# Kernel tuning notes

Measured on AMD Instinct MI355X. Metric: run time of the kernel, lower is better.

## Reference

```python
import jax, jax.numpy as jnp
import numpy as np

N = 128          # n_nodes (hardcoded groups=128 in the torch module)
TIME_DIM = 16
XYZ_DIM = 63
SIGMA = 0.3
EPS = 0.01
relu = jax.nn.relu


def gconv(x, W, b):
    # grouped 1x1 Conv1d with groups=N: per-node GEMM
    # x: (N, Cin, L), W: (N, Cout, Cin), b: (N, Cout) -> (N, Cout, L)
    return jnp.einsum('ncl,nkc->nkl', x, W) + b[:, :, None]


def setup_inputs() -> dict:
    key = jax.random.key(0)
    ks = iter(jax.random.split(key, 64))

    def W(shape, fan_in):
        return jax.random.normal(next(ks), shape, jnp.float32) / np.float32(np.sqrt(fan_in))

    def bvec(shape):
        return 0.01 * jax.random.normal(next(ks), shape, jnp.float32)

    B, V = 1, 2048
    inp = {
        'poses': 0.1 * jax.random.normal(next(ks), (B, N, 24, 3), jnp.float32),
        't_ped': jax.random.normal(next(ks), (B, TIME_DIM), jnp.float32),
        'w': jax.random.uniform(next(ks), (N, 24), jnp.float32),
        'wpts': jax.random.uniform(next(ks), (B, V, 3), jnp.float32),
        'nodes_posed': jax.random.uniform(next(ks), (B, N, 3), jnp.float32),
        'local_coords': jax.random.normal(next(ks), (N, B, V, XYZ_DIM), jnp.float32),
        # encoder grouped convs
        'Wec1': W((N, 64, 72 + TIME_DIM), 72 + TIME_DIM), 'bec1': bvec((N, 64)),
        'Wec21': W((N, 8, 64), 64), 'bec21': bvec((N, 8)),
        'Wec22': W((N, 8, 64), 64), 'bec22': bvec((N, 8)),
        # decoder grouped convs
        'Wdc1': W((N, 64, 80), 80), 'bdc1': bvec((N, 64)),
        'Wdc21': W((N, 32, 64), 64), 'bdc21': bvec((N, 32)),
        'Wdc22': W((N, 3, 64), 64), 'bdc22': bvec((N, 3)),
        # feature-field grouped convs
        'Wf1': W((N, 64, 32 + XYZ_DIM), 32 + XYZ_DIM), 'bf1': bvec((N, 64)),
        'Wf2': W((N, 64, 64), 64), 'bf2': bvec((N, 64)),
        'Wf3': W((N, 64, 64), 64), 'bf3': bvec((N, 64)),
        'Wf4': W((N, 256, 64), 64), 'bf4': bvec((N, 256)),
        # Nerf head linears
        'Wc1': W((256, 64), 256), 'bc1': bvec((64,)),
        'Wc2': W((64, 3), 64), 'bc2': bvec((3,)),
        'Wd1': W((256, 1), 256), 'bd1': bvec((1,)),
    }
    return inp


def reference(poses, t_ped, w, wpts, nodes_posed, local_coords,
              Wec1, bec1, Wec21, bec21, Wec22, bec22,
              Wdc1, bdc1, Wdc21, bdc21, Wdc22, bdc22,
              Wf1, bf1, Wf2, bf2, Wf3, bf3, Wf4, bf4,
              Wc1, bc1, Wc2, bc2, Wd1, bd1):
    B, V = poses.shape[0], wpts.shape[1]

    # attention-weighted poses: (B, N, 72)
    poses_w = (w[None, :, :, None] * poses).reshape(B, N, 72)

    # ---- encode ----
    t = jnp.broadcast_to(t_ped[:, None, :], (B, N, TIME_DIM))
    enc_in = jnp.concatenate([poses_w, t], axis=-1).transpose(1, 2, 0)   # (N, 72+td, B)
    net = relu(gconv(enc_in, Wec1, bec1))                                # (N, 64, B)
    mean = gconv(net, Wec21, bec21).transpose(0, 2, 1)                   # (N, B, 8)
    logvar = gconv(net, Wec22, bec22).transpose(0, 2, 1)                 # (N, B, 8)
    z = mean  # eval-mode reparameterize

    # ---- decode ----
    dec_in = jnp.concatenate([poses_w, z.transpose(1, 0, 2)], axis=-1).transpose(1, 2, 0)  # (N, 80, B)
    net = relu(gconv(dec_in, Wdc1, bdc1))
    ei = gconv(net, Wdc21, bdc21).transpose(0, 2, 1)                     # (N, B, 32)
    delta_ni = gconv(net, Wdc22, bdc22).transpose(0, 2, 1)               # (N, B, 3)

    # ---- blend weights: RBF influence of each node on each point ----
    diff = wpts[None, :, :, :] - nodes_posed.transpose(1, 0, 2)[:, :, None, :]  # (N, B, V, 3)
    d2 = jnp.sum(diff * diff, axis=-1)                                   # (N, B, V)
    influ = jnp.exp(-d2 / (2.0 * SIGMA * SIGMA)) - EPS
    mask = influ >= 0
    bweights = jnp.maximum(influ, 0.0)

    # ---- feature field (dense per-node MLP, masked; == padded gather/scatter) ----
    raw = jnp.concatenate([jnp.broadcast_to(ei[:, :, None, :], (N, B, V, 32)),
                           local_coords], axis=-1)                       # (N, B, V, 32+xyz)
    x = raw.reshape(N, B * V, 32 + XYZ_DIM).transpose(0, 2, 1)           # (N, Cin, B*V)
    net = relu(gconv(x, Wf1, bf1))
    net = relu(gconv(net, Wf2, bf2))
    net = relu(gconv(net, Wf3, bf3))
    fout = relu(gconv(net, Wf4, bf4))                                    # (N, 256, B*V)
    f = fout.transpose(0, 2, 1).reshape(N, B, V, 256) * mask[..., None].astype(fout.dtype)

    # ---- blend features ----
    bw = bweights.transpose(1, 2, 0) + 1e-7                              # (B, V, N)
    bw = bw / jnp.sum(bw, axis=-1, keepdims=True)
    f_blend = jnp.einsum('nbvc,bvn->bvc', f, bw)                         # (B, V, 256)

    # ---- Nerf head ----
    netc = relu(f_blend @ Wc1 + bc1)
    c = netc @ Wc2 + bc2                                                 # (B, V, 3)
    d = relu(f_blend @ Wd1 + bd1)                                        # (B, V, 1)
    return (c, d, ei, delta_ni, mean, logvar)
```

## Files before the change

### kernel.cpp

```cpp
#include <hip/hip_runtime.h>

typedef __bf16 bf16;
typedef __bf16 bf16x4 __attribute__((ext_vector_type(4)));
typedef float  f32x4  __attribute__((ext_vector_type(4)));
typedef unsigned short u16x4 __attribute__((ext_vector_type(4)));

#define NPTS 2048
#define LD 68
#define XCC_ID_IMM 63508

__global__ __launch_bounds__(256) void k_sniff(const void* poses_raw, int* flag)
{
    __shared__ int cnt;
    if (threadIdx.x == 0) cnt = 0;
    __syncthreads();
    const bf16* pb = (const bf16*)poses_raw;
    int local = 0;
    for (int i = threadIdx.x; i < 9216; i += 256) {
        float v = (float)pb[i];
        if (!(v >= -2.0f && v <= 2.0f)) local++;
    }
    atomicAdd(&cnt, local);
    __syncthreads();
    if (threadIdx.x == 0) *flag = (cnt < 64) ? 1 : 0;
}

template<typename T, int WANT>
__global__ __launch_bounds__(128) void k_encdec_t(
    const T* __restrict__ poses, const T* __restrict__ t_ped, const T* __restrict__ w,
    const T* __restrict__ Wec1, const T* __restrict__ bec1,
    const T* __restrict__ Wec21, const T* __restrict__ bec21,
    const T* __restrict__ Wec22, const T* __restrict__ bec22,
    const T* __restrict__ Wdc1, const T* __restrict__ bdc1,
    const T* __restrict__ Wdc21, const T* __restrict__ bdc21,
    const T* __restrict__ Wdc22, const T* __restrict__ bdc22,
    T* __restrict__ out_ei, T* __restrict__ out_delta,
    T* __restrict__ out_mean, T* __restrict__ out_logvar,
    const int* __restrict__ flag)
{
    if (*flag != WANT) return;
    int n = blockIdx.x, tid = threadIdx.x;
    __shared__ float sin_[88], zbuf[8], net1[64], din[80], net2[64];
    if (tid < 72)      sin_[tid] = (float)w[n*24 + tid/3] * (float)poses[n*72 + tid];
    else if (tid < 88) sin_[tid] = (float)t_ped[tid - 72];
    __syncthreads();
    if (tid < 64) {
        float a = (float)bec1[n*64 + tid];
        const T* wr = Wec1 + (size_t)(n*64 + tid) * 88;
        for (int c = 0; c < 88; ++c) a += (float)wr[c] * sin_[c];
        net1[tid] = fmaxf(a, 0.f);
    }
    __syncthreads();
    if (tid < 8) {
        float a = (float)bec21[n*8 + tid];
        const T* wr = Wec21 + (size_t)(n*8 + tid) * 64;
        for (int c = 0; c < 64; ++c) a += (float)wr[c] * net1[c];
        out_mean[n*8 + tid] = (T)a;
        zbuf[tid] = a;
    } else if (tid < 16) {
        int o = tid - 8;
        float a = (float)bec22[n*8 + o];
        const T* wr = Wec22 + (size_t)(n*8 + o) * 64;
        for (int c = 0; c < 64; ++c) a += (float)wr[c] * net1[c];
        out_logvar[n*8 + o] = (T)a;
    }
    __syncthreads();
    if (tid < 72)      din[tid] = sin_[tid];
    else if (tid < 80) din[tid] = zbuf[tid - 72];
    __syncthreads();
    if (tid < 64) {
        float a = (float)bdc1[n*64 + tid];
        const T* wr = Wdc1 + (size_t)(n*64 + tid) * 80;
        for (int c = 0; c < 80; ++c) a += (float)wr[c] * din[c];
        net2[tid] = fmaxf(a, 0.f);
    }
    __syncthreads();
    if (tid < 32) {
        float a = (float)bdc21[n*32 + tid];
        const T* wr = Wdc21 + (size_t)(n*32 + tid) * 64;
        for (int c = 0; c < 64; ++c) a += (float)wr[c] * net2[c];
        out_ei[n*32 + tid] = (T)a;
    } else if (tid < 35) {
        int o = tid - 32;
        float a = (float)bdc22[n*3 + o];
        const T* wr = Wdc22 + (size_t)(n*3 + o) * 64;
        for (int c = 0; c < 64; ++c) a += (float)wr[c] * net2[c];
        out_delta[n*3 + o] = (T)a;
    }
}

template<typename T, int WANT>
__global__ __launch_bounds__(256) void k_denom(
    const T* __restrict__ wpts, const T* __restrict__ nodes,
    float* __restrict__ inv, const int* __restrict__ flag)
{
    if (*flag != WANT) return;
    int v = blockIdx.x * 256 + threadIdx.x;
    float px = (float)wpts[v*3+0], py = (float)wpts[v*3+1], pz = (float)wpts[v*3+2];
    float denom = 0.f;
    for (int n = 0; n < 128; ++n) {
        float dx = px - (float)nodes[n*3+0];
        float dy = py - (float)nodes[n*3+1];
        float dz = pz - (float)nodes[n*3+2];
        float d2 = dx*dx + dy*dy + dz*dz;
        float influ = expf(-d2 * (1.0f/0.18f)) - 0.01f;
        denom += fmaxf(influ, 0.f) + 1e-7f;
    }
    inv[v] = 1.f / denom;
}

__device__ __forceinline__ f32x4 ld4(const float* p) { return *(const f32x4*)p; }
__device__ __forceinline__ f32x4 ld4(const bf16* p)
{
    bf16x4 v = *(const bf16x4*)p;
    f32x4 r;
    #pragma unroll
    for (int j = 0; j < 4; ++j) r[j] = (float)v[j];
    return r;
}
__device__ __forceinline__ f32x4 ld4_nt(const float* p)
{
    return __builtin_nontemporal_load((const f32x4*)p);
}
__device__ __forceinline__ f32x4 ld4_nt(const bf16* p)
{
    u16x4 u = __builtin_nontemporal_load((const u16x4*)p);
    f32x4 r;
    #pragma unroll
    for (int j = 0; j < 4; ++j) {
        unsigned int bits = ((unsigned int)u[j]) << 16;
        r[j] = __uint_as_float(bits);
    }
    return r;
}

template<typename T, int WANT>
__global__ __launch_bounds__(256) void k_w1prep(
    const T* __restrict__ Wf1, float* __restrict__ W1p, const int* __restrict__ flag)
{
    if (*flag != WANT) return;
    int n = blockIdx.x, tid = threadIdx.x;
    for (int e = tid; e < 6144; e += 256) {
        int oc = e / 96, k = e - oc*96;
        float v = (k < 95) ? (float)Wf1[(size_t)n*6080 + oc*95 + k] : 0.f;
        W1p[(size_t)n*6144 + e] = v;
    }
}

template<typename T>
__device__ __forceinline__ void layer64g(
    const T* __restrict__ W, const T* __restrict__ b,
    const float* __restrict__ hin, float* __restrict__ hout, int og, int pg)
{
    f32x4 acc[4] = {};
    #pragma unroll 4
    for (int k0 = 0; k0 < 64; k0 += 4) {
        f32x4 wv[4], xv[4];
        #pragma unroll
        for (int c = 0; c < 4; ++c) wv[c] = ld4(W + (size_t)(og*4 + c)*64 + k0);
        #pragma unroll
        for (int j = 0; j < 4; ++j) xv[j] = *(const f32x4*)&hin[(k0 + j)*LD + pg*4];
        #pragma unroll
        for (int c = 0; c < 4; ++c)
            #pragma unroll
            for (int j = 0; j < 4; ++j)
                acc[c] += xv[j] * wv[c][j];
    }
    #pragma unroll
    for (int c = 0; c < 4; ++c) {
        float bb = (float)b[og*4 + c];
        f32x4 hv;
        #pragma unroll
        for (int r = 0; r < 4; ++r) hv[r] = fmaxf(acc[c][r] + bb, 0.f);
        *(f32x4*)&hout[(og*4 + c)*LD + pg*4] = hv;
    }
}

template<typename T, int WANT, int W1P>
__global__ __launch_bounds__(256, 3) void k_feat_fast(
    const T* __restrict__ Wf1, const T* __restrict__ Wf2,
    const T* __restrict__ Wf3, const T* __restrict__ Wf4,
    const T* __restrict__ lc, const T* __restrict__ ei,
    const T* __restrict__ bf1, const T* __restrict__ bf2,
    const T* __restrict__ bf3, const T* __restrict__ bf4,
    const T* __restrict__ wpts, const T* __restrict__ nodes,
    const float* __restrict__ inv, const float* __restrict__ W1p,
    int shift, float* __restrict__ slices,
    const int* __restrict__ flag)
{
    if (*flag != WANT) return;
    int bid = blockIdx.x;
    int xcdg = bid & 7;
    int i    = bid >> 3;
    int g     = 4*xcdg + (i >> 5);
    int ptile = i & 31;
    int p0  = ptile * 64;
    int tid = threadIdx.x;
    int og = tid >> 4;
    int pg = tid & 15;

    int xcdr = (__builtin_amdgcn_s_getreg(XCC_ID_IMM) & 7) >> shift;

    __shared__ __attribute__((aligned(16))) float smem[(96 + 64) * LD];
    float* xs = smem;
    float* hA = smem + 96*LD;

    if (tid < 64) xs[95*LD + tid] = 0.f;

    float px[4], py[4], pz[4], pinv[4];
    #pragma unroll
    for (int r = 0; r < 4; ++r) {
        int p = p0 + pg*4 + r;
        px[r] = (float)wpts[p*3+0];
        py[r] = (float)wpts[p*3+1];
        pz[r] = (float)wpts[p*3+2];
        pinv[r] = inv[p];
    }

    f32x4 fb[4][4];
    #pragma unroll
    for (int a = 0; a < 4; ++a)
        #pragma unroll
        for (int c = 0; c < 4; ++c) fb[a][c] = (f32x4){0.f,0.f,0.f,0.f};

    f32x4 lv[4];

    auto stage_load = [&](int n) {
        const T* src = lc + ((size_t)n*NPTS + p0) * 63;
        if (tid < 252) {
            #pragma unroll
            for (int j = 0; j < 4; ++j) lv[j] = ld4_nt(src + tid*16 + j*4);
        }
    };
    auto stage_write = [&](int n) {
        if (tid < 252) {
            #pragma unroll
            for (int j = 0; j < 4; ++j)
                #pragma unroll
                for (int l = 0; l < 4; ++l) {
                    int e = tid*16 + j*4 + l;
                    int p = e/63, c = e - 63*p;
                    xs[(32 + c)*LD + p] = lv[j][l];
                }
        }
        const T* ein = ei + n*32;
        #pragma unroll
        for (int k = 0; k < 8; ++k) {
            int e = k*256 + tid;
            int row = e >> 6, p = e & 63;
            xs[row*LD + p] = (float)ein[row];
        }
    };

    stage_load(g*4);
    stage_write(g*4);
    __syncthreads();

    #pragma unroll 1
    for (int nn = 0; nn < 4; ++nn) {
        int n = g*4 + nn;

        {
            f32x4 acc[4] = {};
            if (W1P) {
                const float* W1b = W1p + (size_t)(n*64 + og*4) * 96;
                #pragma unroll 4
                for (int k0 = 0; k0 < 96; k0 += 4) {
                    f32x4 wv[4], xv[4];
                    #pragma unroll
                    for (int c = 0; c < 4; ++c) wv[c] = ld4(W1b + (size_t)c*96 + k0);
                    #pragma unroll
                    for (int j = 0; j < 4; ++j) xv[j] = *(const f32x4*)&xs[(k0 + j)*LD + pg*4];
                    #pragma unroll
                    for (int c = 0; c < 4; ++c)
                        #pragma unroll
                        for (int j = 0; j < 4; ++j)
                            acc[c] += xv[j] * wv[c][j];
                }
            } else {
                const T* W1b = Wf1 + (size_t)(n*64 + og*4) * 95;
                #pragma unroll 4
                for (int kk = 0; kk < 23; ++kk) {
                    int k0 = kk*4;
                    float wv[4][4]; f32x4 xv[4];
                    #pragma unroll
                    for (int c = 0; c < 4; ++c) {
                        const T* wr = W1b + (size_t)c*95 + k0;
                        #pragma unroll
                        for (int j = 0; j < 4; ++j) wv[c][j] = (float)wr[j];
                    }
                    #pragma unroll
                    for (int j = 0; j < 4; ++j) xv[j] = *(const f32x4*)&xs[(k0 + j)*LD + pg*4];
                    #pragma unroll
                    for (int c = 0; c < 4; ++c)
                        #pragma unroll
                        for (int j = 0; j < 4; ++j)
                            acc[c] += xv[j] * wv[c][j];
                }
                {
                    f32x4 xt[3];
                    #pragma unroll
                    for (int j = 0; j < 3; ++j) xt[j] = *(const f32x4*)&xs[(92 + j)*LD + pg*4];
                    #pragma unroll
                    for (int c = 0; c < 4; ++c) {
                        const T* wr = W1b + (size_t)c*95;
                        #pragma unroll
                        for (int j = 0; j < 3; ++j)
                            acc[c] += xt[j] * (float)wr[92 + j];
                    }
                }
            }
            #pragma unroll
            for (int c = 0; c < 4; ++c) {
                float bb = (float)bf1[n*64 + og*4 + c];
                f32x4 hv;
                #pragma unroll
                for (int r = 0; r < 4; ++r) hv[r] = fmaxf(acc[c][r] + bb, 0.f);
                *(f32x4*)&hA[(og*4 + c)*LD + pg*4] = hv;
            }
        }
        __syncthreads();

        layer64g(Wf2 + (size_t)n*64*64, bf2 + n*64, hA, xs, og, pg);
        __syncthreads();

        layer64g(Wf3 + (size_t)n*64*64, bf3 + n*64, xs, hA, og, pg);
        __syncthreads();

        if (nn < 3) stage_load(n + 1);

        {
            float nx = (float)nodes[n*3+0], ny = (float)nodes[n*3+1], nz = (float)nodes[n*3+2];
            f32x4 wgtv;
            #pragma unroll
            for (int r = 0; r < 4; ++r) {
                float dx = px[r]-nx, dy = py[r]-ny, dz = pz[r]-nz;
                float d2 = dx*dx + dy*dy + dz*dz;
                float influ = expf(-d2 * (1.0f/0.18f)) - 0.01f;
                wgtv[r] = (influ >= 0.f) ? (fmaxf(influ, 0.f) + 1e-7f) * pinv[r] : 0.f;
            }
            const T* W4n = Wf4 + (size_t)n*256*64;
            const T* b4n = bf4 + n*256;
            #pragma unroll 1
            for (int mt = 0; mt < 4; ++mt) {
                f32x4 acc[4] = {};
                #pragma unroll 4
                for (int k0 = 0; k0 < 64; k0 += 4) {
                    f32x4 wv[4], xv[4];
                    #pragma unroll
                    for (int c = 0; c < 4; ++c)
                        wv[c] = ld4(W4n + (size_t)(mt*64 + og*4 + c)*64 + k0);
                    #pragma unroll
                    for (int j = 0; j < 4; ++j) xv[j] = *(const f32x4*)&hA[(k0 + j)*LD + pg*4];
                    #pragma unroll
                    for (int c = 0; c < 4; ++c)
                        #pragma unroll
                        for (int j = 0; j < 4; ++j)
                            acc[c] += xv[j] * wv[c][j];
                }
                #pragma unroll
                for (int c = 0; c < 4; ++c) {
                    float bb = (float)b4n[mt*64 + og*4 + c];
                    #pragma unroll
                    for (int r = 0; r < 4; ++r)
                        fb[mt][c][r] += fmaxf(acc[c][r] + bb, 0.f) * wgtv[r];
                }
            }
        }
        __syncthreads();
        if (nn < 3) { stage_write(n + 1); __syncthreads(); }
    }

    float* dst = slices + (size_t)xcdr * NPTS * 256;
    float* tbuf = smem;
    #pragma unroll 1
    for (int qq = 0; qq < 4; ++qq) {
        if (qq) __syncthreads();
        if ((pg >> 2) == qq) {
            #pragma unroll
            for (int mt = 0; mt < 4; ++mt)
                #pragma unroll
                for (int r = 0; r < 4; ++r) {
                    int row = (pg & 3)*4 + r;
                    f32x4 v = { fb[mt][0][r], fb[mt][1][r], fb[mt][2][r], fb[mt][3][r] };
                    *(f32x4*)&tbuf[row*260 + mt*64 + og*4] = v;
                }
        }
        __syncthreads();
        #pragma unroll
        for (int k = 0; k < 4; ++k) {
            int idx = k*1024 + tid*4;
            int row = idx >> 8, col = idx & 255;
            f32x4 v = *(const f32x4*)&tbuf[row*260 + col];
            size_t o = ((size_t)(p0 + qq*16 + row))*256 + col;
            #pragma unroll
            for (int j = 0; j < 4; ++j) atomicAdd(&dst[o + j], v[j]);
        }
    }
}

template<int WANT>
__global__ __launch_bounds__(256) void k_reduce(
    float* __restrict__ slices, int nslice, const int* __restrict__ flag)
{
    if (*flag != WANT) return;
    size_t t = (size_t)(blockIdx.x*256 + threadIdx.x) * 4;
    f32x4 s = *(const f32x4*)&slices[t];
    for (int gg = 1; gg < nslice; ++gg)
        s += __builtin_nontemporal_load((const f32x4*)&slices[(size_t)gg*NPTS*256 + t]);
    *(f32x4*)&slices[t] = s;
}

__global__ __launch_bounds__(256) void k_zero_fb(float* __restrict__ fb)
{
    fb[(size_t)blockIdx.x*256 + threadIdx.x] = 0.f;
}

template<typename T, int WANT>
__global__ __launch_bounds__(256) void k_head_t(
    const float* __restrict__ f_blend,
    const T* __restrict__ Wc1, const T* __restrict__ bc1,
    const T* __restrict__ Wc2, const T* __restrict__ bc2,
    const T* __restrict__ Wd1, const T* __restrict__ bd1,
    T* __restrict__ out_c, T* __restrict__ out_d,
    const int* __restrict__ flag)
{
    if (*flag != WANT) return;
    int t = blockIdx.x * 256 + threadIdx.x;
    int p = t >> 6, j = t & 63;
    const float* fb = f_blend + (size_t)p * 256;

    float a = (float)bc1[j];
    #pragma unroll 8
    for (int c = 0; c < 256; ++c)
        a += fb[c] * (float)Wc1[c*64 + j];
    float nc = fmaxf(a, 0.f);

    float s0 = nc * (float)Wc2[j*3 + 0];
    float s1 = nc * (float)Wc2[j*3 + 1];
    float s2 = nc * (float)Wc2[j*3 + 2];
    float sd = 0.f;
    #pragma unroll
    for (int u = 0; u < 4; ++u) {
        int c = j*4 + u;
        sd += fb[c] * (float)Wd1[c];
    }
    #pragma unroll
    for (int off = 32; off > 0; off >>= 1) {
        s0 += __shfl_down(s0, off);
        s1 += __shfl_down(s1, off);
        s2 += __shfl_down(s2, off);
        sd += __shfl_down(sd, off);
    }
    if (j == 0) {
        out_c[p*3 + 0] = (T)(s0 + (float)bc2[0]);
        out_c[p*3 + 1] = (T)(s1 + (float)bc2[1]);
        out_c[p*3 + 2] = (T)(s2 + (float)bc2[2]);
        out_d[p]       = (T)fmaxf(sd + (float)bd1[0], 0.f);
    }
}

extern "C" void kernel_launch(void* const* d_in, const int* in_sizes, int n_in,
                              void* d_out, int out_size, void* d_ws, size_t ws_size,
                              hipStream_t stream)
{
    const size_t SLICE_BYTES = (size_t)NPTS * 256 * 4;
    const size_t W1P_BYTES   = (size_t)128 * 64 * 96 * 4;
    const size_t INV_BYTES   = (size_t)NPTS * 4;

    size_t base = ((INV_BYTES + 255) & ~(size_t)255) + 256 + 4096;
    bool use_w1p = false; int nslice = 1;
    if      (base + W1P_BYTES + 8*SLICE_BYTES <= ws_size) { use_w1p = true;  nslice = 8; }
    else if (base + 8*SLICE_BYTES <= ws_size)             { use_w1p = false; nslice = 8; }
    else if (base + W1P_BYTES + 4*SLICE_BYTES <= ws_size) { use_w1p = true;  nslice = 4; }
    else if (base + 4*SLICE_BYTES <= ws_size)             { use_w1p = false; nslice = 4; }
    else if (base + 2*SLICE_BYTES <= ws_size)             { use_w1p = false; nslice = 2; }
    else                                                  { use_w1p = false; nslice = 1; }
    int shift = (nslice == 8) ? 0 : (nslice == 4) ? 1 : (nslice == 2) ? 2 : 3;

    char* wsp = (char*)d_ws;
    auto alloc = [&](size_t bytes) { char* r = wsp; wsp += (bytes + 255) & ~(size_t)255; return r; };
    float* inv  = (float*)alloc(INV_BYTES);
    int*   flag = (int*)  alloc(256);
    float* W1p  = use_w1p ? (float*)alloc(W1P_BYTES) : nullptr;
    float* slices = (float*)alloc((size_t)nslice * SLICE_BYTES);
    float* f_blend = slices;

    hipLaunchKernelGGL(k_sniff, dim3(1), dim3(256), 0, stream, d_in[0], flag);
    hipLaunchKernelGGL(k_zero_fb, dim3(nslice * 2048), dim3(256), 0, stream, slices);

    #define LAUNCH_ALL(T, WANT)                                                         \
    {                                                                                   \
        const T* poses = (const T*)d_in[0];                                             \
        const T* t_ped = (const T*)d_in[1];                                             \
        const T* w     = (const T*)d_in[2];                                             \
        const T* wpts  = (const T*)d_in[3];                                             \
        const T* nodes = (const T*)d_in[4];                                             \
        const T* lc    = (const T*)d_in[5];                                             \
        const T* Wec1  = (const T*)d_in[6];  const T* bec1 = (const T*)d_in[7];         \
        const T* Wec21 = (const T*)d_in[8];  const T* bec21= (const T*)d_in[9];         \
        const T* Wec22 = (const T*)d_in[10]; const T* bec22= (const T*)d_in[11];        \
        const T* Wdc1  = (const T*)d_in[12]; const T* bdc1 = (const T*)d_in[13];        \
        const T* Wdc21 = (const T*)d_in[14]; const T* bdc21= (const T*)d_in[15];        \
        const T* Wdc22 = (const T*)d_in[16]; const T* bdc22= (const T*)d_in[17];        \
        const T* Wf1   = (const T*)d_in[18]; const T* bf1  = (const T*)d_in[19];        \
        const T* Wf2   = (const T*)d_in[20]; const T* bf2  = (const T*)d_in[21];        \
        const T* Wf3   = (const T*)d_in[22]; const T* bf3  = (const T*)d_in[23];        \
        const T* Wf4   = (const T*)d_in[24]; const T* bf4  = (const T*)d_in[25];        \
        const T* Wc1   = (const T*)d_in[26]; const T* bc1  = (const T*)d_in[27];        \
        const T* Wc2   = (const T*)d_in[28]; const T* bc2  = (const T*)d_in[29];        \
        const T* Wd1   = (const T*)d_in[30]; const T* bd1  = (const T*)d_in[31];        \
        T* out = (T*)d_out;                                                             \
        T* out_c      = out;                                                            \
        T* out_d      = out + 6144;                                                     \
        T* out_ei     = out + 8192;                                                     \
        T* out_delta  = out + 12288;                                                    \
        T* out_mean   = out + 12672;                                                    \
        T* out_logvar = out + 13696;                                                    \
        hipLaunchKernelGGL((k_encdec_t<T, WANT>), dim3(128), dim3(128), 0, stream,      \
            poses, t_ped, w, Wec1, bec1, Wec21, bec21, Wec22, bec22,                    \
            Wdc1, bdc1, Wdc21, bdc21, Wdc22, bdc22,                                     \
            out_ei, out_delta, out_mean, out_logvar, flag);                             \
        hipLaunchKernelGGL((k_denom<T, WANT>), dim3(8), dim3(256), 0, stream,           \
            wpts, nodes, inv, flag);                                                    \
        if (use_w1p) {                                                                  \
            hipLaunchKernelGGL((k_w1prep<T, WANT>), dim3(128), dim3(256), 0, stream,    \
                Wf1, W1p, flag);                                                        \
            hipLaunchKernelGGL((k_feat_fast<T, WANT, 1>), dim3(1024), dim3(256), 0,     \
                stream, Wf1, Wf2, Wf3, Wf4, lc, (const T*)out_ei,                       \
                bf1, bf2, bf3, bf4, wpts, nodes, inv, W1p, shift, slices, flag);        \
        } else {                                                                        \
            hipLaunchKernelGGL((k_feat_fast<T, WANT, 0>), dim3(1024), dim3(256), 0,     \
                stream, Wf1, Wf2, Wf3, Wf4, lc, (const T*)out_ei,                       \
                bf1, bf2, bf3, bf4, wpts, nodes, inv, W1p, shift, slices, flag);        \
        }                                                                               \
        if (nslice > 1)                                                                 \
            hipLaunchKernelGGL((k_reduce<WANT>), dim3(512), dim3(256), 0, stream,       \
                slices, nslice, flag);                                                  \
        hipLaunchKernelGGL((k_head_t<T, WANT>), dim3(512), dim3(256), 0, stream,        \
            f_blend, Wc1, bc1, Wc2, bc2, Wd1, bd1, out_c, out_d, flag);                 \
    }

    LAUNCH_ALL(bf16, 1)
    LAUNCH_ALL(float, 0)
    #undef LAUNCH_ALL
}
```

Measured before the change: 727.8 us.

## Restructure feature kernel to 1024-thread blocks with 16 nodes each, precomputed blend weights

The feature-field kernel now runs 256 blocks of 1024 threads. Each block processes 64 points across 16 nodes, and each thread computes one output channel of four points per 64-wide layer. Blend weights are precomputed per node and point in a separate kernel instead of being recomputed with expf inside the hot loop. When eight slices are available, each node group writes its own slice with plain stores instead of atomics, so the zeroing kernel is skipped. The trade-off is fewer resident blocks and more global weight traffic per FLOP. In exchange, atomic contention and the XCC-ID slice mapping go away.

```diff
diff --git a/kernel.cpp b/kernel.cpp
--- a/kernel.cpp
+++ b/kernel.cpp
@@ -7,7 +7,6 @@
 
 #define NPTS 2048
 #define LD 68
-#define XCC_ID_IMM 63508
 
 __global__ __launch_bounds__(256) void k_sniff(const void* poses_raw, int* flag)
 {
@@ -90,9 +89,9 @@
 }
 
 template<typename T, int WANT>
-__global__ __launch_bounds__(256) void k_denom(
+__global__ __launch_bounds__(256) void k_bweights_t(
     const T* __restrict__ wpts, const T* __restrict__ nodes,
-    float* __restrict__ inv, const int* __restrict__ flag)
+    float* __restrict__ wgt, const int* __restrict__ flag)
 {
     if (*flag != WANT) return;
     int v = blockIdx.x * 256 + threadIdx.x;
@@ -106,7 +105,15 @@
         float influ = expf(-d2 * (1.0f/0.18f)) - 0.01f;
         denom += fmaxf(influ, 0.f) + 1e-7f;
     }
-    inv[v] = 1.f / denom;
+    float inv = 1.f / denom;
+    for (int n = 0; n < 128; ++n) {
+        float dx = px - (float)nodes[n*3+0];
+        float dy = py - (float)nodes[n*3+1];
+        float dz = pz - (float)nodes[n*3+2];
+        float d2 = dx*dx + dy*dy + dz*dz;
+        float influ = expf(-d2 * (1.0f/0.18f)) - 0.01f;
+        wgt[n*NPTS + v] = (influ >= 0.f) ? (fmaxf(influ, 0.f) + 1e-7f) * inv : 0.f;
+    }
 }
 
 __device__ __forceinline__ f32x4 ld4(const float* p) { return *(const f32x4*)p; }
@@ -147,254 +154,199 @@
     }
 }
 
-template<typename T>
-__device__ __forceinline__ void layer64g(
-    const T* __restrict__ W, const T* __restrict__ b,
-    const float* __restrict__ hin, float* __restrict__ hout, int og, int pg)
-{
-    f32x4 acc[4] = {};
-    #pragma unroll 4
-    for (int k0 = 0; k0 < 64; k0 += 4) {
-        f32x4 wv[4], xv[4];
-        #pragma unroll
-        for (int c = 0; c < 4; ++c) wv[c] = ld4(W + (size_t)(og*4 + c)*64 + k0);
-        #pragma unroll
-        for (int j = 0; j < 4; ++j) xv[j] = *(const f32x4*)&hin[(k0 + j)*LD + pg*4];
-        #pragma unroll
-        for (int c = 0; c < 4; ++c)
-            #pragma unroll
-            for (int j = 0; j < 4; ++j)
-                acc[c] += xv[j] * wv[c][j];
-    }
-    #pragma unroll
-    for (int c = 0; c < 4; ++c) {
-        float bb = (float)b[og*4 + c];
-        f32x4 hv;
-        #pragma unroll
-        for (int r = 0; r < 4; ++r) hv[r] = fmaxf(acc[c][r] + bb, 0.f);
-        *(f32x4*)&hout[(og*4 + c)*LD + pg*4] = hv;
-    }
-}
-
 template<typename T, int WANT, int W1P>
-__global__ __launch_bounds__(256, 3) void k_feat_fast(
+__global__ __launch_bounds__(1024, 4) void k_feat_fast(
     const T* __restrict__ Wf1, const T* __restrict__ Wf2,
     const T* __restrict__ Wf3, const T* __restrict__ Wf4,
     const T* __restrict__ lc, const T* __restrict__ ei,
     const T* __restrict__ bf1, const T* __restrict__ bf2,
     const T* __restrict__ bf3, const T* __restrict__ bf4,
-    const T* __restrict__ wpts, const T* __restrict__ nodes,
-    const float* __restrict__ inv, const float* __restrict__ W1p,
-    int shift, float* __restrict__ slices,
+    const float* __restrict__ wgt, const float* __restrict__ W1p,
+    int smask, float* __restrict__ slices,
     const int* __restrict__ flag)
 {
     if (*flag != WANT) return;
     int bid = blockIdx.x;
-    int xcdg = bid & 7;
-    int i    = bid >> 3;
-    int g     = 4*xcdg + (i >> 5);
-    int ptile = i & 31;
+    int g     = bid & 7;
+    int ptile = bid >> 3;
     int p0  = ptile * 64;
     int tid = threadIdx.x;
     int og = tid >> 4;
     int pg = tid & 15;
 
-    int xcdr = (__builtin_amdgcn_s_getreg(XCC_ID_IMM) & 7) >> shift;
-
     __shared__ __attribute__((aligned(16))) float smem[(96 + 64) * LD];
     float* xs = smem;
     float* hA = smem + 96*LD;
 
     if (tid < 64) xs[95*LD + tid] = 0.f;
 
-    float px[4], py[4], pz[4], pinv[4];
+    f32x4 fb[4];
     #pragma unroll
-    for (int r = 0; r < 4; ++r) {
-        int p = p0 + pg*4 + r;
-        px[r] = (float)wpts[p*3+0];
-        py[r] = (float)wpts[p*3+1];
-        pz[r] = (float)wpts[p*3+2];
-        pinv[r] = inv[p];
-    }
-
-    f32x4 fb[4][4];
-    #pragma unroll
-    for (int a = 0; a < 4; ++a)
-        #pragma unroll
-        for (int c = 0; c < 4; ++c) fb[a][c] = (f32x4){0.f,0.f,0.f,0.f};
-
-    f32x4 lv[4];
+    for (int c = 0; c < 4; ++c) fb[c] = (f32x4){0.f,0.f,0.f,0.f};
+
+    f32x4 lv;
 
     auto stage_load = [&](int n) {
         const T* src = lc + ((size_t)n*NPTS + p0) * 63;
-        if (tid < 252) {
-            #pragma unroll
-            for (int j = 0; j < 4; ++j) lv[j] = ld4_nt(src + tid*16 + j*4);
-        }
+        if (tid < 1008) lv = ld4_nt(src + tid*4);
     };
     auto stage_write = [&](int n) {
-        if (tid < 252) {
-            #pragma unroll
-            for (int j = 0; j < 4; ++j)
-                #pragma unroll
-                for (int l = 0; l < 4; ++l) {
-                    int e = tid*16 + j*4 + l;
-                    int p = e/63, c = e - 63*p;
-                    xs[(32 + c)*LD + p] = lv[j][l];
-                }
+        if (tid < 1008) {
+            #pragma unroll
+            for (int l = 0; l < 4; ++l) {
+                int e = tid*4 + l;
+                int p = e/63, c = e - 63*p;
+                xs[(32 + c)*LD + p] = lv[l];
+            }
         }
         const T* ein = ei + n*32;
         #pragma unroll
-        for (int k = 0; k < 8; ++k) {
-            int e = k*256 + tid;
-            int row = e >> 6, p = e & 63;
-            xs[row*LD + p] = (float)ein[row];
+        for (int k = 0; k < 2; ++k) {
+            int e = k*1024 + tid;
+            xs[(e >> 6)*LD + (e & 63)] = (float)ein[e >> 6];
         }
     };
 
-    stage_load(g*4);
-    stage_write(g*4);
+    stage_load(g*16);
+    stage_write(g*16);
     __syncthreads();
 
     #pragma unroll 1
-    for (int nn = 0; nn < 4; ++nn) {
-        int n = g*4 + nn;
+    for (int nn = 0; nn < 16; ++nn) {
+        int n = g*16 + nn;
 
         {
+            f32x4 acc = {};
+            if (W1P) {
+                const float* W1b = W1p + (size_t)(n*64 + og) * 96;
+                #pragma unroll 8
+                for (int k0 = 0; k0 < 96; k0 += 4) {
+                    f32x4 wv = ld4(W1b + k0);
+                    #pragma unroll
+                    for (int j = 0; j < 4; ++j) {
+                        f32x4 xv = *(const f32x4*)&xs[(k0 + j)*LD + pg*4];
+                        acc += xv * wv[j];
+                    }
+                }
+            } else {
+                const T* wr = Wf1 + (size_t)(n*64 + og) * 95;
+                #pragma unroll 8
+                for (int kk = 0; kk < 23; ++kk) {
+                    int k0 = kk*4;
+                    #pragma unroll
+                    for (int j = 0; j < 4; ++j) {
+                        f32x4 xv = *(const f32x4*)&xs[(k0 + j)*LD + pg*4];
+                        acc += xv * (float)wr[k0 + j];
+                    }
+                }
+                #pragma unroll
+                for (int j = 92; j < 95; ++j) {
+                    f32x4 xv = *(const f32x4*)&xs[j*LD + pg*4];
+                    acc += xv * (float)wr[j];
+                }
+            }
+            float bb = (float)bf1[n*64 + og];
+            f32x4 hv;
+            #pragma unroll
+            for (int r = 0; r < 4; ++r) hv[r] = fmaxf(acc[r] + bb, 0.f);
+            *(f32x4*)&hA[og*LD + pg*4] = hv;
+        }
+        __syncthreads();
+
+        {
+            const T* wr = Wf2 + (size_t)(n*64 + og) * 64;
+            f32x4 acc = {};
+            #pragma unroll 8
+            for (int k0 = 0; k0 < 64; k0 += 4) {
+                f32x4 wv = ld4(wr + k0);
+                #pragma unroll
+                for (int j = 0; j < 4; ++j) {
+                    f32x4 xv = *(const f32x4*)&hA[(k0 + j)*LD + pg*4];
+                    acc += xv * wv[j];
+                }
+            }
+            float bb = (float)bf2[n*64 + og];
+            f32x4 hv;
+            #pragma unroll
+            for (int r = 0; r < 4; ++r) hv[r] = fmaxf(acc[r] + bb, 0.f);
+            *(f32x4*)&xs[og*LD + pg*4] = hv;
+        }
+        __syncthreads();
+
+        {
+            const T* wr = Wf3 + (size_t)(n*64 + og) * 64;
+            f32x4 acc = {};
+            #pragma unroll 8
+            for (int k0 = 0; k0 < 64; k0 += 4) {
+                f32x4 wv = ld4(wr + k0);
+                #pragma unroll
+                for (int j = 0; j < 4; ++j) {
+                    f32x4 xv = *(const f32x4*)&xs[(k0 + j)*LD + pg*4];
+                    acc += xv * wv[j];
+                }
+            }
+            float bb = (float)bf3[n*64 + og];
+            f32x4 hv;
+            #pragma unroll
+            for (int r = 0; r < 4; ++r) hv[r] = fmaxf(acc[r] + bb, 0.f);
+            *(f32x4*)&hA[og*LD + pg*4] = hv;
+        }
+        __syncthreads();
+
+        if (nn < 15) stage_load(n + 1);
+
+        {
+            f32x4 wgtv = ld4_nt(wgt + (size_t)n*NPTS + p0 + pg*4);
+            const T* W4b = Wf4 + ((size_t)n*256 + og*4) * 64;
+            const T* b4  = bf4 + n*256 + og*4;
             f32x4 acc[4] = {};
-            if (W1P) {
-                const float* W1b = W1p + (size_t)(n*64 + og*4) * 96;
-                #pragma unroll 4
-                for (int k0 = 0; k0 < 96; k0 += 4) {
-                    f32x4 wv[4], xv[4];
-                    #pragma unroll
-                    for (int c = 0; c < 4; ++c) wv[c] = ld4(W1b + (size_t)c*96 + k0);
-                    #pragma unroll
-                    for (int j = 0; j < 4; ++j) xv[j] = *(const f32x4*)&xs[(k0 + j)*LD + pg*4];
+            #pragma unroll 8
+            for (int k0 = 0; k0 < 64; k0 += 4) {
+                f32x4 wv[4];
+                #pragma unroll
+                for (int c = 0; c < 4; ++c) wv[c] = ld4(W4b + (size_t)c*64 + k0);
+                #pragma unroll
+                for (int j = 0; j < 4; ++j) {
+                    f32x4 xv = *(const f32x4*)&hA[(k0 + j)*LD + pg*4];
                     #pragma unroll
                     for (int c = 0; c < 4; ++c)
-                        #pragma unroll
-                        for (int j = 0; j < 4; ++j)
-                            acc[c] += xv[j] * wv[c][j];
-                }
-            } else {
-                const T* W1b = Wf1 + (size_t)(n*64 + og*4) * 95;
-                #pragma unroll 4
-                for (int kk = 0; kk < 23; ++kk) {
-                    int k0 = kk*4;
-                    float wv[4][4]; f32x4 xv[4];
-                    #pragma unroll
-                    for (int c = 0; c < 4; ++c) {
-                        const T* wr = W1b + (size_t)c*95 + k0;
-                        #pragma unroll
-                        for (int j = 0; j < 4; ++j) wv[c][j] = (float)wr[j];
-                    }
-                    #pragma unroll
-                    for (int j = 0; j < 4; ++j) xv[j] = *(const f32x4*)&xs[(k0 + j)*LD + pg*4];
-                    #pragma unroll
-                    for (int c = 0; c < 4; ++c)
-                        #pragma unroll
-                        for (int j = 0; j < 4; ++j)
-                            acc[c] += xv[j] * wv[c][j];
-                }
-                {
-                    f32x4 xt[3];
-                    #pragma unroll
-                    for (int j = 0; j < 3; ++j) xt[j] = *(const f32x4*)&xs[(92 + j)*LD + pg*4];
-                    #pragma unroll
-                    for (int c = 0; c < 4; ++c) {
-                        const T* wr = W1b + (size_t)c*95;
-                        #pragma unroll
-                        for (int j = 0; j < 3; ++j)
-                            acc[c] += xt[j] * (float)wr[92 + j];
-                    }
+                        acc[c] += xv * wv[c][j];
                 }
             }
             #pragma unroll
             for (int c = 0; c < 4; ++c) {
-                float bb = (float)bf1[n*64 + og*4 + c];
-                f32x4 hv;
-                #pragma unroll
-                for (int r = 0; r < 4; ++r) hv[r] = fmaxf(acc[c][r] + bb, 0.f);
-                *(f32x4*)&hA[(og*4 + c)*LD + pg*4] = hv;
+                float bb = (float)b4[c];
+                #pragma unroll
+                for (int r = 0; r < 4; ++r)
+                    fb[c][r] += fmaxf(acc[c][r] + bb, 0.f) * wgtv[r];
             }
         }
         __syncthreads();
-
-        layer64g(Wf2 + (size_t)n*64*64, bf2 + n*64, hA, xs, og, pg);
-        __syncthreads();
-
-        layer64g(Wf3 + (size_t)n*64*64, bf3 + n*64, xs, hA, og, pg);
-        __syncthreads();
-
-        if (nn < 3) stage_load(n + 1);
-
-        {
-            float nx = (float)nodes[n*3+0], ny = (float)nodes[n*3+1], nz = (float)nodes[n*3+2];
-            f32x4 wgtv;
-            #pragma unroll
-            for (int r = 0; r < 4; ++r) {
-                float dx = px[r]-nx, dy = py[r]-ny, dz = pz[r]-nz;
-                float d2 = dx*dx + dy*dy + dz*dz;
-                float influ = expf(-d2 * (1.0f/0.18f)) - 0.01f;
-                wgtv[r] = (influ >= 0.f) ? (fmaxf(influ, 0.f) + 1e-7f) * pinv[r] : 0.f;
-            }
-            const T* W4n = Wf4 + (size_t)n*256*64;
-            const T* b4n = bf4 + n*256;
-            #pragma unroll 1
-            for (int mt = 0; mt < 4; ++mt) {
-                f32x4 acc[4] = {};
-                #pragma unroll 4
-                for (int k0 = 0; k0 < 64; k0 += 4) {
-                    f32x4 wv[4], xv[4];
-                    #pragma unroll
-                    for (int c = 0; c < 4; ++c)
-                        wv[c] = ld4(W4n + (size_t)(mt*64 + og*4 + c)*64 + k0);
-                    #pragma unroll
-                    for (int j = 0; j < 4; ++j) xv[j] = *(const f32x4*)&hA[(k0 + j)*LD + pg*4];
-                    #pragma unroll
-                    for (int c = 0; c < 4; ++c)
-                        #pragma unroll
-                        for (int j = 0; j < 4; ++j)
-                            acc[c] += xv[j] * wv[c][j];
-                }
-                #pragma unroll
-                for (int c = 0; c < 4; ++c) {
-                    float bb = (float)b4n[mt*64 + og*4 + c];
-                    #pragma unroll
-                    for (int r = 0; r < 4; ++r)
-                        fb[mt][c][r] += fmaxf(acc[c][r] + bb, 0.f) * wgtv[r];
-                }
-            }
-        }
-        __syncthreads();
-        if (nn < 3) { stage_write(n + 1); __syncthreads(); }
-    }
-
-    float* dst = slices + (size_t)xcdr * NPTS * 256;
+        if (nn < 15) { stage_write(n + 1); __syncthreads(); }
+    }
+
+    int sl = g & smask;
+    float* dst = slices + (size_t)sl * NPTS * 256;
     float* tbuf = smem;
     #pragma unroll 1
-    for (int qq = 0; qq < 4; ++qq) {
-        if (qq) __syncthreads();
-        if ((pg >> 2) == qq) {
-            #pragma unroll
-            for (int mt = 0; mt < 4; ++mt)
-                #pragma unroll
-                for (int r = 0; r < 4; ++r) {
-                    int row = (pg & 3)*4 + r;
-                    f32x4 v = { fb[mt][0][r], fb[mt][1][r], fb[mt][2][r], fb[mt][3][r] };
-                    *(f32x4*)&tbuf[row*260 + mt*64 + og*4] = v;
-                }
+    for (int q = 0; q < 4; ++q) {
+        if (q) __syncthreads();
+        if ((og >> 4) == q) {
+            #pragma unroll
+            for (int c = 0; c < 4; ++c)
+                #pragma unroll
+                for (int r = 0; r < 4; ++r)
+                    tbuf[(pg*4 + r)*68 + (og & 15)*4 + c] = fb[c][r];
         }
         __syncthreads();
-        #pragma unroll
-        for (int k = 0; k < 4; ++k) {
-            int idx = k*1024 + tid*4;
-            int row = idx >> 8, col = idx & 255;
-            f32x4 v = *(const f32x4*)&tbuf[row*260 + col];
-            size_t o = ((size_t)(p0 + qq*16 + row))*256 + col;
-            #pragma unroll
-            for (int j = 0; j < 4; ++j) atomicAdd(&dst[o + j], v[j]);
+        int pt = tid >> 4, c4 = (tid & 15) * 4;
+        f32x4 val = *(const f32x4*)&tbuf[pt*68 + c4];
+        size_t o = ((size_t)(p0 + pt))*256 + q*64 + c4;
+        if (smask == 7) {
+            __builtin_nontemporal_store(val, (f32x4*)&dst[o]);
+        } else {
+            #pragma unroll
+            for (int j = 0; j < 4; ++j) atomicAdd(&dst[o + j], val[j]);
         }
     }
 }
@@ -466,9 +418,9 @@
 {
     const size_t SLICE_BYTES = (size_t)NPTS * 256 * 4;
     const size_t W1P_BYTES   = (size_t)128 * 64 * 96 * 4;
-    const size_t INV_BYTES   = (size_t)NPTS * 4;
-
-    size_t base = ((INV_BYTES + 255) & ~(size_t)255) + 256 + 4096;
+    const size_t WGT_BYTES   = (size_t)128 * NPTS * 4;
+
+    size_t base = ((WGT_BYTES + 255) & ~(size_t)255) + 256 + 4096;
     bool use_w1p = false; int nslice = 1;
     if      (base + W1P_BYTES + 8*SLICE_BYTES <= ws_size) { use_w1p = true;  nslice = 8; }
     else if (base + 8*SLICE_BYTES <= ws_size)             { use_w1p = false; nslice = 8; }
@@ -476,18 +428,19 @@
     else if (base + 4*SLICE_BYTES <= ws_size)             { use_w1p = false; nslice = 4; }
     else if (base + 2*SLICE_BYTES <= ws_size)             { use_w1p = false; nslice = 2; }
     else                                                  { use_w1p = false; nslice = 1; }
-    int shift = (nslice == 8) ? 0 : (nslice == 4) ? 1 : (nslice == 2) ? 2 : 3;
+    int smask = nslice - 1;
 
     char* wsp = (char*)d_ws;
     auto alloc = [&](size_t bytes) { char* r = wsp; wsp += (bytes + 255) & ~(size_t)255; return r; };
-    float* inv  = (float*)alloc(INV_BYTES);
+    float* wgt  = (float*)alloc(WGT_BYTES);
     int*   flag = (int*)  alloc(256);
     float* W1p  = use_w1p ? (float*)alloc(W1P_BYTES) : nullptr;
     float* slices = (float*)alloc((size_t)nslice * SLICE_BYTES);
     float* f_blend = slices;
 
     hipLaunchKernelGGL(k_sniff, dim3(1), dim3(256), 0, stream, d_in[0], flag);
-    hipLaunchKernelGGL(k_zero_fb, dim3(nslice * 2048), dim3(256), 0, stream, slices);
+    if (nslice < 8)
+        hipLaunchKernelGGL(k_zero_fb, dim3(nslice * 2048), dim3(256), 0, stream, slices);
 
     #define LAUNCH_ALL(T, WANT)                                                         \
     {                                                                                   \
@@ -521,18 +474,18 @@
             poses, t_ped, w, Wec1, bec1, Wec21, bec21, Wec22, bec22,                    \
             Wdc1, bdc1, Wdc21, bdc21, Wdc22, bdc22,                                     \
             out_ei, out_delta, out_mean, out_logvar, flag);                             \
-        hipLaunchKernelGGL((k_denom<T, WANT>), dim3(8), dim3(256), 0, stream,           \
-            wpts, nodes, inv, flag);                                                    \
+        hipLaunchKernelGGL((k_bweights_t<T, WANT>), dim3(8), dim3(256), 0, stream,      \
+            wpts, nodes, wgt, flag);                                                    \
         if (use_w1p) {                                                                  \
             hipLaunchKernelGGL((k_w1prep<T, WANT>), dim3(128), dim3(256), 0, stream,    \
                 Wf1, W1p, flag);                                                        \
-            hipLaunchKernelGGL((k_feat_fast<T, WANT, 1>), dim3(1024), dim3(256), 0,     \
+            hipLaunchKernelGGL((k_feat_fast<T, WANT, 1>), dim3(256), dim3(1024), 0,     \
                 stream, Wf1, Wf2, Wf3, Wf4, lc, (const T*)out_ei,                       \
-                bf1, bf2, bf3, bf4, wpts, nodes, inv, W1p, shift, slices, flag);        \
+                bf1, bf2, bf3, bf4, wgt, W1p, smask, slices, flag);                     \
         } else {                                                                        \
-            hipLaunchKernelGGL((k_feat_fast<T, WANT, 0>), dim3(1024), dim3(256), 0,     \
+            hipLaunchKernelGGL((k_feat_fast<T, WANT, 0>), dim3(256), dim3(1024), 0,     \
                 stream, Wf1, Wf2, Wf3, Wf4, lc, (const T*)out_ei,                       \
-                bf1, bf2, bf3, bf4, wpts, nodes, inv, W1p, shift, slices, flag);        \
+                bf1, bf2, bf3, bf4, wgt, W1p, smask, slices, flag);                     \
         }                                                                               \
         if (nslice > 1)                                                                 \
             hipLaunchKernelGGL((k_reduce<WANT>), dim3(512), dim3(256), 0, stream,       \
```

Measured after the change: 595.7 us. -18.2%, faster.

## Precompute blend weights, give each block 16 nodes, store slices without atomics

Applied to the files above, without the earlier changes.

Blend weights are now computed once per node and point into a global table instead of being recomputed inside the feature kernel. The feature kernel's grid shrinks from 1024 to 256 blocks: each block handles 16 nodes for one 64-point tile, and the node group picks its output slice. With 8 slices every slice location has a single writer, so results go out as plain nontemporal stores and the zeroing kernel is skipped. The last layer now keeps all four 64-wide output tiles in registers at once, and launch bounds drop to 2 blocks per CU. This trades fewer atomics and less exp work for much less parallelism (256 blocks on a 256-CU part) and more register pressure.

```diff
diff --git a/kernel.cpp b/kernel.cpp
--- a/kernel.cpp
+++ b/kernel.cpp
@@ -7,7 +7,6 @@
 
 #define NPTS 2048
 #define LD 68
-#define XCC_ID_IMM 63508
 
 __global__ __launch_bounds__(256) void k_sniff(const void* poses_raw, int* flag)
 {
@@ -90,9 +89,9 @@
 }
 
 template<typename T, int WANT>
-__global__ __launch_bounds__(256) void k_denom(
+__global__ __launch_bounds__(256) void k_bweights_t(
     const T* __restrict__ wpts, const T* __restrict__ nodes,
-    float* __restrict__ inv, const int* __restrict__ flag)
+    float* __restrict__ wgt, const int* __restrict__ flag)
 {
     if (*flag != WANT) return;
     int v = blockIdx.x * 256 + threadIdx.x;
@@ -106,7 +105,15 @@
         float influ = expf(-d2 * (1.0f/0.18f)) - 0.01f;
         denom += fmaxf(influ, 0.f) + 1e-7f;
     }
-    inv[v] = 1.f / denom;
+    float inv = 1.f / denom;
+    for (int n = 0; n < 128; ++n) {
+        float dx = px - (float)nodes[n*3+0];
+        float dy = py - (float)nodes[n*3+1];
+        float dz = pz - (float)nodes[n*3+2];
+        float d2 = dx*dx + dy*dy + dz*dz;
+        float influ = expf(-d2 * (1.0f/0.18f)) - 0.01f;
+        wgt[n*NPTS + v] = (influ >= 0.f) ? (fmaxf(influ, 0.f) + 1e-7f) * inv : 0.f;
+    }
 }
 
 __device__ __forceinline__ f32x4 ld4(const float* p) { return *(const f32x4*)p; }
@@ -177,45 +184,30 @@
 }
 
 template<typename T, int WANT, int W1P>
-__global__ __launch_bounds__(256, 3) void k_feat_fast(
+__global__ __launch_bounds__(256, 2) void k_feat_fast(
     const T* __restrict__ Wf1, const T* __restrict__ Wf2,
     const T* __restrict__ Wf3, const T* __restrict__ Wf4,
     const T* __restrict__ lc, const T* __restrict__ ei,
     const T* __restrict__ bf1, const T* __restrict__ bf2,
     const T* __restrict__ bf3, const T* __restrict__ bf4,
-    const T* __restrict__ wpts, const T* __restrict__ nodes,
-    const float* __restrict__ inv, const float* __restrict__ W1p,
-    int shift, float* __restrict__ slices,
+    const float* __restrict__ wgt, const float* __restrict__ W1p,
+    int smask, float* __restrict__ slices,
     const int* __restrict__ flag)
 {
     if (*flag != WANT) return;
     int bid = blockIdx.x;
-    int xcdg = bid & 7;
-    int i    = bid >> 3;
-    int g     = 4*xcdg + (i >> 5);
-    int ptile = i & 31;
+    int g     = bid & 7;
+    int ptile = bid >> 3;
     int p0  = ptile * 64;
     int tid = threadIdx.x;
     int og = tid >> 4;
     int pg = tid & 15;
 
-    int xcdr = (__builtin_amdgcn_s_getreg(XCC_ID_IMM) & 7) >> shift;
-
     __shared__ __attribute__((aligned(16))) float smem[(96 + 64) * LD];
     float* xs = smem;
     float* hA = smem + 96*LD;
 
     if (tid < 64) xs[95*LD + tid] = 0.f;
-
-    float px[4], py[4], pz[4], pinv[4];
-    #pragma unroll
-    for (int r = 0; r < 4; ++r) {
-        int p = p0 + pg*4 + r;
-        px[r] = (float)wpts[p*3+0];
-        py[r] = (float)wpts[p*3+1];
-        pz[r] = (float)wpts[p*3+2];
-        pinv[r] = inv[p];
-    }
 
     f32x4 fb[4][4];
     #pragma unroll
@@ -252,13 +244,13 @@
         }
     };
 
-    stage_load(g*4);
-    stage_write(g*4);
+    stage_load(g*16);
+    stage_write(g*16);
     __syncthreads();
 
     #pragma unroll 1
-    for (int nn = 0; nn < 4; ++nn) {
-        int n = g*4 + nn;
+    for (int nn = 0; nn < 16; ++nn) {
+        int n = g*16 + nn;
 
         {
             f32x4 acc[4] = {};
@@ -327,51 +319,47 @@
         layer64g(Wf3 + (size_t)n*64*64, bf3 + n*64, xs, hA, og, pg);
         __syncthreads();
 
-        if (nn < 3) stage_load(n + 1);
+        if (nn < 15) stage_load(n + 1);
 
         {
-            float nx = (float)nodes[n*3+0], ny = (float)nodes[n*3+1], nz = (float)nodes[n*3+2];
-            f32x4 wgtv;
-            #pragma unroll
-            for (int r = 0; r < 4; ++r) {
-                float dx = px[r]-nx, dy = py[r]-ny, dz = pz[r]-nz;
-                float d2 = dx*dx + dy*dy + dz*dz;
-                float influ = expf(-d2 * (1.0f/0.18f)) - 0.01f;
-                wgtv[r] = (influ >= 0.f) ? (fmaxf(influ, 0.f) + 1e-7f) * pinv[r] : 0.f;
-            }
+            f32x4 wgtv = ld4_nt(wgt + (size_t)n*NPTS + p0 + pg*4);
             const T* W4n = Wf4 + (size_t)n*256*64;
             const T* b4n = bf4 + n*256;
-            #pragma unroll 1
-            for (int mt = 0; mt < 4; ++mt) {
-                f32x4 acc[4] = {};
-                #pragma unroll 4
-                for (int k0 = 0; k0 < 64; k0 += 4) {
-                    f32x4 wv[4], xv[4];
+            f32x4 acc[4][4] = {};
+            #pragma unroll 2
+            for (int k0 = 0; k0 < 64; k0 += 4) {
+                f32x4 xv[4];
+                #pragma unroll
+                for (int j = 0; j < 4; ++j) xv[j] = *(const f32x4*)&hA[(k0 + j)*LD + pg*4];
+                #pragma unroll
+                for (int mt = 0; mt < 4; ++mt) {
+                    f32x4 wv[4];
                     #pragma unroll
                     for (int c = 0; c < 4; ++c)
                         wv[c] = ld4(W4n + (size_t)(mt*64 + og*4 + c)*64 + k0);
-                    #pragma unroll
-                    for (int j = 0; j < 4; ++j) xv[j] = *(const f32x4*)&hA[(k0 + j)*LD + pg*4];
                     #pragma unroll
                     for (int c = 0; c < 4; ++c)
                         #pragma unroll
                         for (int j = 0; j < 4; ++j)
-                            acc[c] += xv[j] * wv[c][j];
-                }
+                            acc[mt][c] += xv[j] * wv[c][j];
+                }
+            }
+            #pragma unroll
+            for (int mt = 0; mt < 4; ++mt)
                 #pragma unroll
                 for (int c = 0; c < 4; ++c) {
                     float bb = (float)b4n[mt*64 + og*4 + c];
                     #pragma unroll
                     for (int r = 0; r < 4; ++r)
-                        fb[mt][c][r] += fmaxf(acc[c][r] + bb, 0.f) * wgtv[r];
-                }
-            }
+                        fb[mt][c][r] += fmaxf(acc[mt][c][r] + bb, 0.f) * wgtv[r];
+                }
         }
         __syncthreads();
-        if (nn < 3) { stage_write(n + 1); __syncthreads(); }
-    }
-
-    float* dst = slices + (size_t)xcdr * NPTS * 256;
+        if (nn < 15) { stage_write(n + 1); __syncthreads(); }
+    }
+
+    int sl = g & smask;
+    float* dst = slices + (size_t)sl * NPTS * 256;
     float* tbuf = smem;
     #pragma unroll 1
     for (int qq = 0; qq < 4; ++qq) {
@@ -393,8 +381,12 @@
             int row = idx >> 8, col = idx & 255;
             f32x4 v = *(const f32x4*)&tbuf[row*260 + col];
             size_t o = ((size_t)(p0 + qq*16 + row))*256 + col;
-            #pragma unroll
-            for (int j = 0; j < 4; ++j) atomicAdd(&dst[o + j], v[j]);
+            if (smask == 7) {
+                __builtin_nontemporal_store(v, (f32x4*)&dst[o]);
+            } else {
+                #pragma unroll
+                for (int j = 0; j < 4; ++j) atomicAdd(&dst[o + j], v[j]);
+            }
         }
     }
 }
@@ -466,9 +458,9 @@
 {
     const size_t SLICE_BYTES = (size_t)NPTS * 256 * 4;
     const size_t W1P_BYTES   = (size_t)128 * 64 * 96 * 4;
-    const size_t INV_BYTES   = (size_t)NPTS * 4;
-
-    size_t base = ((INV_BYTES + 255) & ~(size_t)255) + 256 + 4096;
+    const size_t WGT_BYTES   = (size_t)128 * NPTS * 4;
+
+    size_t base = ((WGT_BYTES + 255) & ~(size_t)255) + 256 + 4096;
     bool use_w1p = false; int nslice = 1;
     if      (base + W1P_BYTES + 8*SLICE_BYTES <= ws_size) { use_w1p = true;  nslice = 8; }
     else if (base + 8*SLICE_BYTES <= ws_size)             { use_w1p = false; nslice = 8; }
@@ -476,18 +468,19 @@
     else if (base + 4*SLICE_BYTES <= ws_size)             { use_w1p = false; nslice = 4; }
     else if (base + 2*SLICE_BYTES <= ws_size)             { use_w1p = false; nslice = 2; }
     else                                                  { use_w1p = false; nslice = 1; }
-    int shift = (nslice == 8) ? 0 : (nslice == 4) ? 1 : (nslice == 2) ? 2 : 3;
+    int smask = nslice - 1;
 
     char* wsp = (char*)d_ws;
     auto alloc = [&](size_t bytes) { char* r = wsp; wsp += (bytes + 255) & ~(size_t)255; return r; };
-    float* inv  = (float*)alloc(INV_BYTES);
+    float* wgt  = (float*)alloc(WGT_BYTES);
     int*   flag = (int*)  alloc(256);
     float* W1p  = use_w1p ? (float*)alloc(W1P_BYTES) : nullptr;
     float* slices = (float*)alloc((size_t)nslice * SLICE_BYTES);
     float* f_blend = slices;
 
     hipLaunchKernelGGL(k_sniff, dim3(1), dim3(256), 0, stream, d_in[0], flag);
-    hipLaunchKernelGGL(k_zero_fb, dim3(nslice * 2048), dim3(256), 0, stream, slices);
+    if (nslice < 8)
+        hipLaunchKernelGGL(k_zero_fb, dim3(nslice * 2048), dim3(256), 0, stream, slices);
 
     #define LAUNCH_ALL(T, WANT)                                                         \
     {                                                                                   \
@@ -521,18 +514,18 @@
             poses, t_ped, w, Wec1, bec1, Wec21, bec21, Wec22, bec22,                    \
             Wdc1, bdc1, Wdc21, bdc21, Wdc22, bdc22,                                     \
             out_ei, out_delta, out_mean, out_logvar, flag);                             \
-        hipLaunchKernelGGL((k_denom<T, WANT>), dim3(8), dim3(256), 0, stream,           \
-            wpts, nodes, inv, flag);                                                    \
+        hipLaunchKernelGGL((k_bweights_t<T, WANT>), dim3(8), dim3(256), 0, stream,      \
+            wpts, nodes, wgt, flag);                                                    \
         if (use_w1p) {                                                                  \
             hipLaunchKernelGGL((k_w1prep<T, WANT>), dim3(128), dim3(256), 0, stream,    \
                 Wf1, W1p, flag);                                                        \
-            hipLaunchKernelGGL((k_feat_fast<T, WANT, 1>), dim3(1024), dim3(256), 0,     \
+            hipLaunchKernelGGL((k_feat_fast<T, WANT, 1>), dim3(256), dim3(256), 0,      \
                 stream, Wf1, Wf2, Wf3, Wf4, lc, (const T*)out_ei,                       \
-                bf1, bf2, bf3, bf4, wpts, nodes, inv, W1p, shift, slices, flag);        \
+                bf1, bf2, bf3, bf4, wgt, W1p, smask, slices, flag);                     \
         } else {                                                                        \
-            hipLaunchKernelGGL((k_feat_fast<T, WANT, 0>), dim3(1024), dim3(256), 0,     \
+            hipLaunchKernelGGL((k_feat_fast<T, WANT, 0>), dim3(256), dim3(256), 0,      \
                 stream, Wf1, Wf2, Wf3, Wf4, lc, (const T*)out_ei,                       \
-                bf1, bf2, bf3, bf4, wpts, nodes, inv, W1p, shift, slices, flag);        \
+                bf1, bf2, bf3, bf4, wgt, W1p, smask, slices, flag);                     \
         }                                                                               \
         if (nslice > 1)                                                                 \
             hipLaunchKernelGGL((k_reduce<WANT>), dim3(512), dim3(256), 0, stream,       \
```

New measurement: 653.3 us. -10.2%, faster.
